# Optimization experiments

Measured on AMD Instinct MI355X. Metric: run time of the kernel, lower is better.

Reference implementation:

```python
import jax, jax.numpy as jnp
import numpy as np

WIN_LEN = 5
RES_LEN = None


def _log_sparse_mask(Q_L, K_L, win_len=0, res_len=None):
    # Faithful port of LogSparseMask (numpy, static shapes -> constant-folded under jit)
    if res_len is None:
        L_ls = K_L - 1 - win_len
        n_reps = 1
    else:
        n_reps = int(np.ceil(K_L / res_len))
        L_ls = res_len
    l_floor = int(np.log2(L_ls))
    indxs = np.array([int(2 ** (l_floor - i)) for i in range(l_floor + 1)])
    reps_array = np.expand_dims(np.arange(n_reps, dtype='int') * L_ls, 1)
    indxs = (indxs + reps_array + win_len).flatten()
    indxs = indxs[indxs < K_L - 1]
    my_mask = np.ones(K_L, dtype='int')
    my_mask[indxs] = 0
    my_mask[:win_len + 1] = 0
    my_mask = np.concatenate([np.flip(my_mask[1:]), my_mask])
    my_mask = np.array([my_mask[K_L - i:K_L * 2 - i] for i in range(1, Q_L + 1)], dtype=bool)
    return my_mask  # [Q_L, K_L], True = masked out


def _combined_mask(L, S):
    causal = np.triu(np.ones((L, S), dtype=bool), k=1)  # TriangularCausalMask
    sparse = _log_sparse_mask(L, S, WIN_LEN, RES_LEN)
    return jnp.asarray(causal | sparse)[None, None]  # [1,1,L,S], broadcasts over B,H


def setup_inputs() -> dict:
    key = jax.random.key(0)
    k1, k2, k3 = jax.random.split(key, 3)
    B, L, H, E, D = 4, 2048, 8, 64, 64
    return {
        'queries': jax.random.normal(k1, (B, L, H, E), dtype=jnp.float32),
        'keys': jax.random.normal(k2, (B, L, H, E), dtype=jnp.float32),
        'values': jax.random.normal(k3, (B, L, H, D), dtype=jnp.float32),
    }


def reference(queries, keys, values):
    B, L, H, E = queries.shape
    S = keys.shape[1]
    scale = 1.0 / np.sqrt(E)  # self.scale is None -> 1/sqrt(E)
    # [B,H,L,S] full score matrix (eager), then causal|log-sparse masked_fill(-inf)
    scores = jnp.einsum('blhe,bshe->bhls', queries, keys)
    mask = _combined_mask(L, S)
    scores = jnp.where(mask, -jnp.inf, scale * scores)
    A = jax.nn.softmax(scores, axis=-1)  # dropout p=0.0 (eval) -> identity
    V = jnp.einsum('bhls,bshd->blhd', A, values)
    return V  # module returns (V, None); attention weights not output
```

## Files before the change

kernel.cpp:

```cpp
#include <hip/hip_runtime.h>
#include <stdint.h>


static constexpr int Bn = 4, Ln = 2048, Hn = 8, En = 64;
static constexpr int NDELTA = 17;

__global__ __launch_bounds__(256) void logsparse_attn_kernel(
    const float* __restrict__ Q,
    const float* __restrict__ K,
    const float* __restrict__ V,
    float* __restrict__ O)
{
    constexpr int deltas[NDELTA] = {0,1,2,3,4,5,6,7,9,13,21,37,69,133,261,517,1029};

    const int t   = blockIdx.x * 256 + threadIdx.x;
    const int sub = t & 15;
    const int qid = t >> 4;
    const int q   = qid & (Ln - 1);
    const int bh  = qid >> 11;
    const int b   = bh >> 3;
    const int h   = bh & 7;

    const size_t bhBase = ((size_t)b * Ln * Hn + (size_t)h) * (size_t)En;
    const size_t rowQ   = bhBase + (size_t)q * (Hn * En);

    float4 qv = *(const float4*)(Q + rowQ + sub * 4);
    qv.x *= 0.125f; qv.y *= 0.125f; qv.z *= 0.125f; qv.w *= 0.125f;

    float sc[NDELTA];
    #pragma unroll
    for (int d = 0; d < NDELTA; ++d) {
        const int j  = q - deltas[d];
        const int jc = (j < 0) ? 0 : j;
        const float4 kv = *(const float4*)(K + bhBase + (size_t)jc * (Hn * En) + sub * 4);
        float s = qv.x * kv.x + qv.y * kv.y + qv.z * kv.z + qv.w * kv.w;
        s += __shfl_xor(s, 1);
        s += __shfl_xor(s, 2);
        s += __shfl_xor(s, 4);
        s += __shfl_xor(s, 8);
        sc[d] = (j < 0) ? -__builtin_inff() : s;
    }

    float m = sc[0];
    #pragma unroll
    for (int d = 1; d < NDELTA; ++d) m = fmaxf(m, sc[d]);
    float p[NDELTA];
    float sum = 0.0f;
    #pragma unroll
    for (int d = 0; d < NDELTA; ++d) {
        p[d] = __expf(sc[d] - m);
        sum += p[d];
    }
    const float inv = 1.0f / sum;

    float ax = 0.f, ay = 0.f, az = 0.f, aw = 0.f;
    #pragma unroll
    for (int d = 0; d < NDELTA; ++d) {
        const int j  = q - deltas[d];
        const int jc = (j < 0) ? 0 : j;
        const float4 vv = *(const float4*)(V + bhBase + (size_t)jc * (Hn * En) + sub * 4);
        const float w = p[d];
        ax = fmaf(w, vv.x, ax);
        ay = fmaf(w, vv.y, ay);
        az = fmaf(w, vv.z, az);
        aw = fmaf(w, vv.w, aw);
    }

    float4 o;
    o.x = ax * inv; o.y = ay * inv; o.z = az * inv; o.w = aw * inv;
    *(float4*)(O + rowQ + sub * 4) = o;
}

extern "C" void kernel_launch(void* const* d_in, const int* in_sizes, int n_in,
                              void* d_out, int out_size, void* d_ws, size_t ws_size,
                              hipStream_t stream) {
    const float* Q = (const float*)d_in[0];
    const float* K = (const float*)d_in[1];
    const float* V = (const float*)d_in[2];
    float* O = (float*)d_out;

    const int total_threads = Bn * Hn * Ln * 16;
    logsparse_attn_kernel<<<total_threads / 256, 256, 0, stream>>>(Q, K, V, O);
}
```

Measured before the change: 103.8 us.

## Use 8 threads per query and interleave blocks across batch-heads

Each query row is now handled by 8 threads with two float4 loads each instead of 16 threads with one. This cuts the shuffle reduction by one step and halves the thread count. Blocks are also remapped so consecutive block indices cycle over the 32 batch-head pairs, which changes the order in which K/V rows are touched and could affect L2 locality. In exchange each thread keeps more registers live and there is less thread-level parallelism to hide memory latency.

```diff
diff --git a/kernel.cpp b/kernel.cpp
--- a/kernel.cpp
+++ b/kernel.cpp
@@ -13,31 +13,36 @@
 {
     constexpr int deltas[NDELTA] = {0,1,2,3,4,5,6,7,9,13,21,37,69,133,261,517,1029};
 
-    const int t   = blockIdx.x * 256 + threadIdx.x;
-    const int sub = t & 15;
-    const int qid = t >> 4;
-    const int q   = qid & (Ln - 1);
-    const int bh  = qid >> 11;
-    const int b   = bh >> 3;
-    const int h   = bh & 7;
+    const int bh = blockIdx.x & 31;
+    const int l  = blockIdx.x >> 5;
+    const int b  = bh >> 3;
+    const int h  = bh & 7;
+
+    const int sub = threadIdx.x & 7;
+    const int q   = l * 32 + (threadIdx.x >> 3);
 
     const size_t bhBase = ((size_t)b * Ln * Hn + (size_t)h) * (size_t)En;
     const size_t rowQ   = bhBase + (size_t)q * (Hn * En);
+    const int    dimOff = sub * 8;
 
-    float4 qv = *(const float4*)(Q + rowQ + sub * 4);
-    qv.x *= 0.125f; qv.y *= 0.125f; qv.z *= 0.125f; qv.w *= 0.125f;
+    const float4 q0 = *(const float4*)(Q + rowQ + dimOff);
+    const float4 q1 = *(const float4*)(Q + rowQ + dimOff + 4);
+    float qf[8] = { q0.x*0.125f, q0.y*0.125f, q0.z*0.125f, q0.w*0.125f,
+                    q1.x*0.125f, q1.y*0.125f, q1.z*0.125f, q1.w*0.125f };
 
     float sc[NDELTA];
     #pragma unroll
     for (int d = 0; d < NDELTA; ++d) {
         const int j  = q - deltas[d];
         const int jc = (j < 0) ? 0 : j;
-        const float4 kv = *(const float4*)(K + bhBase + (size_t)jc * (Hn * En) + sub * 4);
-        float s = qv.x * kv.x + qv.y * kv.y + qv.z * kv.z + qv.w * kv.w;
+        const float* kp = K + bhBase + (size_t)jc * (Hn * En) + dimOff;
+        const float4 k0 = *(const float4*)(kp);
+        const float4 k1 = *(const float4*)(kp + 4);
+        float s = qf[0]*k0.x + qf[1]*k0.y + qf[2]*k0.z + qf[3]*k0.w
+                + qf[4]*k1.x + qf[5]*k1.y + qf[6]*k1.z + qf[7]*k1.w;
         s += __shfl_xor(s, 1);
         s += __shfl_xor(s, 2);
         s += __shfl_xor(s, 4);
-        s += __shfl_xor(s, 8);
         sc[d] = (j < 0) ? -__builtin_inff() : s;
     }
 
@@ -53,22 +58,30 @@
     }
     const float inv = 1.0f / sum;
 
-    float ax = 0.f, ay = 0.f, az = 0.f, aw = 0.f;
+    float acc[8] = {0,0,0,0,0,0,0,0};
     #pragma unroll
     for (int d = 0; d < NDELTA; ++d) {
         const int j  = q - deltas[d];
         const int jc = (j < 0) ? 0 : j;
-        const float4 vv = *(const float4*)(V + bhBase + (size_t)jc * (Hn * En) + sub * 4);
+        const float* vp = V + bhBase + (size_t)jc * (Hn * En) + dimOff;
+        const float4 v0 = *(const float4*)(vp);
+        const float4 v1 = *(const float4*)(vp + 4);
         const float w = p[d];
-        ax = fmaf(w, vv.x, ax);
-        ay = fmaf(w, vv.y, ay);
-        az = fmaf(w, vv.z, az);
-        aw = fmaf(w, vv.w, aw);
+        acc[0] = fmaf(w, v0.x, acc[0]);
+        acc[1] = fmaf(w, v0.y, acc[1]);
+        acc[2] = fmaf(w, v0.z, acc[2]);
+        acc[3] = fmaf(w, v0.w, acc[3]);
+        acc[4] = fmaf(w, v1.x, acc[4]);
+        acc[5] = fmaf(w, v1.y, acc[5]);
+        acc[6] = fmaf(w, v1.z, acc[6]);
+        acc[7] = fmaf(w, v1.w, acc[7]);
     }
 
-    float4 o;
-    o.x = ax * inv; o.y = ay * inv; o.z = az * inv; o.w = aw * inv;
-    *(float4*)(O + rowQ + sub * 4) = o;
+    float4 o0, o1;
+    o0.x = acc[0]*inv; o0.y = acc[1]*inv; o0.z = acc[2]*inv; o0.w = acc[3]*inv;
+    o1.x = acc[4]*inv; o1.y = acc[5]*inv; o1.z = acc[6]*inv; o1.w = acc[7]*inv;
+    *(float4*)(O + rowQ + dimOff)     = o0;
+    *(float4*)(O + rowQ + dimOff + 4) = o1;
 }
 
 extern "C" void kernel_launch(void* const* d_in, const int* in_sizes, int n_in,
@@ -79,6 +92,6 @@
     const float* V = (const float*)d_in[2];
     float* O = (float*)d_out;
 
-    const int total_threads = Bn * Hn * Ln * 16;
+    const int total_threads = Bn * Hn * Ln * 8;
     logsparse_attn_kernel<<<total_threads / 256, 256, 0, stream>>>(Q, K, V, O);
 }
```

New measurement: 107.7 us. 3.7% more time.
